# Kernel optimization log

Measured on AMD Instinct MI355X. Metric: run time of the kernel, lower is better.

## Reference

```python
import jax, jax.numpy as jnp
import numpy as np


def setup_inputs() -> dict:
    key = jax.random.key(0)
    x = jax.random.normal(key, (4096, 16384), dtype=jnp.float32)
    return {"x": x, "k": 256}


def reference(x, k):
    # Faithful to Get_Top_K: top_k over abs(x) per row, then scatter the
    # (abs) top-k VALUES back into a zero tensor at their original columns.
    vals, idx = jax.lax.top_k(jnp.abs(x), k)          # [B, K], [B, K]
    rows = jnp.arange(x.shape[0])[:, None]             # [B, 1] broadcast to [B, K]
    out = jnp.zeros_like(x).at[rows, idx].set(vals)    # scatter_nd equivalent
    return out
```

## Files before the change

### kernel.cpp

```cpp
#include <hip/hip_runtime.h>

#define COLS 16384
#define TPB  1024
#define NV   4
#define NW   (TPB / 64)
#define NBIN 4096
#define CHK  (NBIN / TPB)
#define SH1  12
#define RPB  2

typedef unsigned uvec4 __attribute__((ext_vector_type(4)));
typedef float    fvec4 __attribute__((ext_vector_type(4)));

__global__ __launch_bounds__(TPB, 8) void topk_abs_kernel(
    const float* __restrict__ x, const int* __restrict__ kp,
    float* __restrict__ out, int rows)
{
    __shared__ int      hist[NBIN];
    __shared__ int      wsum[NW];
    __shared__ unsigned s_cnt, s_max, s_total;
    __shared__ int      s_bin, s_G, s_eq;

    const int tid = threadIdx.x, lane = tid & 63, wid = tid >> 6;
    const int row0 = blockIdx.x * RPB;
    const int kin = kp[0];
    const unsigned kk = (unsigned)(kin < 0 ? 0 : (kin > COLS ? COLS : kin));

    const uvec4* __restrict__ xrA = (const uvec4*)(x + (size_t)row0 * COLS);
    const uvec4* __restrict__ xrB = (const uvec4*)(x + (size_t)(row0 + 1) * COLS);
    fvec4* __restrict__ orA = (fvec4*)(out + (size_t)row0 * COLS);
    fvec4* __restrict__ orB = (fvec4*)(out + (size_t)(row0 + 1) * COLS);
    const bool hasB = (row0 + 1) < rows;

    uvec4 ubA[NV], ubB[NV];
    #pragma unroll
    for (int i = 0; i < NV; ++i) ubA[i] = xrA[i * TPB + tid];
    if (hasB) {
        #pragma unroll
        for (int i = 0; i < NV; ++i) ubB[i] = xrB[i * TPB + tid];
    }
    #pragma unroll
    for (int j = 0; j < CHK; ++j) hist[tid + j * TPB] = 0;
    __syncthreads();

    auto scan_pick = [&](int rank) {
        const int c  = (TPB - 1) - tid;
        const int b0 = c * CHK;
        int S = 0;
        #pragma unroll
        for (int j = 0; j < CHK; ++j) S += hist[b0 + j];
        int P = S;
        #pragma unroll
        for (int d = 1; d < 64; d <<= 1) { int t = __shfl_up(P, d); if (lane >= d) P += t; }
        if (lane == 63) wsum[wid] = P;
        __syncthreads();
        for (int w = 0; w < wid; ++w) P += wsum[w];
        const int above = P - S;
        if (P >= rank && above < rank) {
            int cum = above;
            #pragma unroll
            for (int j = CHK - 1; j >= 0; --j) {
                int h = hist[b0 + j], prev = cum;
                cum += h;
                if (cum >= rank && prev < rank) { s_bin = b0 + j; s_G = prev; s_eq = h; }
            }
        }
        if (tid == TPB - 1) s_total = (unsigned)P;
        __syncthreads();
    };

    const unsigned T0 = 0x3FE66666u;

    auto process = [&](uvec4 (&ub)[NV], fvec4* __restrict__ or4, bool prep_next) {
        #pragma unroll
        for (int i = 0; i < NV; ++i) {
            uvec4 t = ub[i] & 0x7FFFFFFFu;
            ub[i] = t;
            #define H1(u) { if ((u) >= T0) { unsigned b = ((u) - T0) >> SH1; \
                            b = b < (NBIN - 1) ? b : (NBIN - 1); atomicAdd(&hist[b], 1); } }
            H1(t.x) H1(t.y) H1(t.z) H1(t.w)
            #undef H1
        }
        __syncthreads();

        unsigned T = 0xFFFFFFFFu;
        int need = 0, eq = 0;
        if (kk > 0) {
            scan_pick((int)kk);
            const unsigned cnt = s_total;
            const int B1 = s_bin, G1 = s_G, E1 = s_eq;
            bool handled = false;
            if (cnt == kk) { T = T0; need = 0; eq = 0; handled = true; }
            else if (cnt > kk && B1 < NBIN - 1) {
                if (G1 + E1 == (int)kk) {
                    T = T0 + ((unsigned)B1 << SH1); need = 0; eq = 0; handled = true;
                } else {
                    const unsigned A1 = T0 + ((unsigned)B1 << SH1);
                    const int r1 = (int)kk - G1;
                    #pragma unroll
                    for (int j = 0; j < CHK; ++j) hist[tid + j * TPB] = 0;
                    __syncthreads();
                    #pragma unroll
                    for (int i = 0; i < NV; ++i) {
                        #define H2(u) { unsigned d = (u) - A1; if (d < (unsigned)NBIN) atomicAdd(&hist[d], 1); }
                        H2(ub[i].x) H2(ub[i].y) H2(ub[i].z) H2(ub[i].w)
                        #undef H2
                    }
                    __syncthreads();
                    scan_pick(r1);
                    T = A1 + (unsigned)s_bin; need = r1 - s_G; eq = s_eq;
                    handled = true;
                }
            }
            if (!handled) {
                if (tid == 0) s_max = 0u;
                __syncthreads();
                unsigned lmax = 0u;
                #pragma unroll
                for (int i = 0; i < NV; ++i)
                    lmax = max(lmax, max(max(ub[i].x, ub[i].y), max(ub[i].z, ub[i].w)));
                #pragma unroll
                for (int d = 32; d; d >>= 1) lmax = max(lmax, (unsigned)__shfl_xor((int)lmax, d));
                if (lane == 0) atomicMax(&s_max, lmax);
                __syncthreads();
                const unsigned smax = s_max;

                auto count_ge = [&](unsigned Tq) -> unsigned {
                    __syncthreads();
                    if (tid == 0) s_cnt = 0;
                    __syncthreads();
                    int c = 0;
                    #pragma unroll
                    for (int i = 0; i < NV; ++i)
                        c += (ub[i].x >= Tq) + (ub[i].y >= Tq) + (ub[i].z >= Tq) + (ub[i].w >= Tq);
                    #pragma unroll
                    for (int d = 32; d; d >>= 1) c += __shfl_xor(c, d);
                    if (lane == 0) atomicAdd(&s_cnt, (unsigned)c);
                    __syncthreads();
                    return s_cnt;
                };

                unsigned T0f = T0, cntf = (kk > 0) ? s_total : 0u;
                if (cntf < kk) {
                    unsigned lo = 0u, hi = T0;
                    while (hi - lo > 1u) {
                        unsigned mid = lo + ((hi - lo) >> 1);
                        if (count_ge(mid) >= kk) lo = mid; else hi = mid;
                    }
                    T0f = lo;
                    cntf = count_ge(T0f);
                }
                if (cntf == kk)       { T = T0f; need = 0; eq = 0; }
                else if (smax == T0f) { T = T0f; eq = (int)cntf; need = (int)kk; }
                else {
                    const unsigned range = smax - T0f;
                    const int topbit = 31 - __clz(range);
                    int sh = topbit - 7; if (sh < 0) sh = 0;
                    unsigned A = T0f;
                    unsigned W = (topbit >= 31) ? 0xFFFFFFFFu : (1u << (topbit + 1));
                    int r = (int)kk;
                    for (;;) {
                        if (tid < 256) hist[tid] = 0;
                        __syncthreads();
                        #pragma unroll
                        for (int i = 0; i < NV; ++i) {
                            #define HR(u) { if ((u) >= A && ((u) - A) < W) atomicAdd(&hist[((u) - A) >> sh], 1); }
                            HR(ub[i].x) HR(ub[i].y) HR(ub[i].z) HR(ub[i].w)
                            #undef HR
                        }
                        __syncthreads();
                        int bin = 0, val = 0, s = 0;
                        if (tid < 256) {
                            bin = 255 - tid;
                            val = hist[bin];
                            s = val;
                            #pragma unroll
                            for (int d = 1; d < 64; d <<= 1) { int t = __shfl_up(s, d); if (lane >= d) s += t; }
                            if (lane == 63) wsum[wid] = s;
                        }
                        __syncthreads();
                        if (tid < 256) {
                            for (int w = 0; w < wid; ++w) s += wsum[w];
                            if (s >= r && (s - val) < r) { s_bin = bin; s_G = s - val; if (sh == 0) s_eq = val; }
                        }
                        __syncthreads();
                        A += ((unsigned)s_bin) << sh;
                        W = 1u << sh;
                        r -= s_G;
                        if (sh == 0) break;
                        sh = (sh >= 8) ? sh - 8 : 0;
                    }
                    T = A; need = r; eq = s_eq;
                }
            }
        }

        unsigned cstar = COLS - 1;
        if (kk > 0 && need != eq) {
            unsigned loC = 0, hiC = COLS - 1;
            while (loC < hiC) {
                unsigned mid = (loC + hiC) >> 1;
                __syncthreads();
                if (tid == 0) s_cnt = 0;
                __syncthreads();
                int c = 0;
                #pragma unroll
                for (int i = 0; i < NV; ++i) {
                    const unsigned cb = (unsigned)(i * TPB + tid) * 4u;
                    c += (ub[i].x == T && (cb + 0) <= mid);
                    c += (ub[i].y == T && (cb + 1) <= mid);
                    c += (ub[i].z == T && (cb + 2) <= mid);
                    c += (ub[i].w == T && (cb + 3) <= mid);
                }
                #pragma unroll
                for (int d = 32; d; d >>= 1) c += __shfl_xor(c, d);
                if (lane == 0) atomicAdd(&s_cnt, (unsigned)c);
                __syncthreads();
                if (s_cnt >= (unsigned)need) hiC = mid; else loC = mid + 1;
            }
            cstar = loC;
        }

        if (prep_next) {
            #pragma unroll
            for (int j = 0; j < CHK; ++j) hist[tid + j * TPB] = 0;
        }

        #pragma unroll
        for (int i = 0; i < NV; ++i) {
            const unsigned cb = (unsigned)(i * TPB + tid) * 4u;
            const unsigned u0 = ub[i].x, u1 = ub[i].y, u2 = ub[i].z, u3 = ub[i].w;
            fvec4 o;
            o.x = (u0 > T || (u0 == T && (cb + 0) <= cstar)) ? __uint_as_float(u0) : 0.f;
            o.y = (u1 > T || (u1 == T && (cb + 1) <= cstar)) ? __uint_as_float(u1) : 0.f;
            o.z = (u2 > T || (u2 == T && (cb + 2) <= cstar)) ? __uint_as_float(u2) : 0.f;
            o.w = (u3 > T || (u3 == T && (cb + 3) <= cstar)) ? __uint_as_float(u3) : 0.f;
            __builtin_nontemporal_store(o, &or4[i * TPB + tid]);
        }
        if (prep_next) __syncthreads();
    };

    process(ubA, orA, hasB);
    if (hasB) process(ubB, orB, false);
}

extern "C" void kernel_launch(void* const* d_in, const int* in_sizes, int n_in,
                              void* d_out, int out_size, void* d_ws, size_t ws_size,
                              hipStream_t stream)
{
    const float* x   = (const float*)d_in[0];
    const int*   kp  = (const int*)d_in[1];
    float*       out = (float*)d_out;
    int rows = in_sizes[0] / COLS;
    int grid = (rows + RPB - 1) / RPB;
    topk_abs_kernel<<<grid, TPB, 0, stream>>>(x, kp, out, rows);
}
```

Measured before the change: 81.79 us.

## Process both rows' radix-select passes jointly with packed dual-histogram scans

Instead of running the full select pipeline for row A and then for row B, both rows now build their histograms into separate shared buffers at the same time. A single scan packs the two 16-bit counts into one 32-bit prefix sum. The refinement pass is also shared between the rows, which roughly halves the barrier-bound phases per block. In exchange it doubles histogram shared memory to 32KB, which may lower occupancy against the 8-blocks launch bound, and it relies on per-row counts fitting in 16 bits (max 16384 fits).

```diff
diff --git a/kernel.cpp b/kernel.cpp
--- a/kernel.cpp
+++ b/kernel.cpp
@@ -16,10 +16,12 @@
     const float* __restrict__ x, const int* __restrict__ kp,
     float* __restrict__ out, int rows)
 {
-    __shared__ int      hist[NBIN];
+    __shared__ int      hist[2][NBIN];
+    __shared__ unsigned wsum2[NW];
     __shared__ int      wsum[NW];
-    __shared__ unsigned s_cnt, s_max, s_total;
-    __shared__ int      s_bin, s_G, s_eq;
+    __shared__ unsigned s_cnt, s_max;
+    __shared__ unsigned s_total[2];
+    __shared__ int      s_bin[2], s_G[2], s_eq[2];
 
     const int tid = threadIdx.x, lane = tid & 63, wid = tid >> 6;
     const int row0 = blockIdx.x * RPB;
@@ -40,208 +42,253 @@
         for (int i = 0; i < NV; ++i) ubB[i] = xrB[i * TPB + tid];
     }
     #pragma unroll
-    for (int j = 0; j < CHK; ++j) hist[tid + j * TPB] = 0;
+    for (int j = 0; j < CHK; ++j) { hist[0][tid + j * TPB] = 0; hist[1][tid + j * TPB] = 0; }
     __syncthreads();
 
-    auto scan_pick = [&](int rank) {
+    const unsigned T0 = 0x3FE66666u;
+
+    #pragma unroll
+    for (int i = 0; i < NV; ++i) {
+        uvec4 t = ubA[i] & 0x7FFFFFFFu; ubA[i] = t;
+        #define H1(u) { if ((u) >= T0) { unsigned b = ((u) - T0) >> SH1; \
+                        b = b < (NBIN - 1) ? b : (NBIN - 1); atomicAdd(&hist[0][b], 1); } }
+        H1(t.x) H1(t.y) H1(t.z) H1(t.w)
+        #undef H1
+    }
+    if (hasB) {
+        #pragma unroll
+        for (int i = 0; i < NV; ++i) {
+            uvec4 t = ubB[i] & 0x7FFFFFFFu; ubB[i] = t;
+            #define H1(u) { if ((u) >= T0) { unsigned b = ((u) - T0) >> SH1; \
+                            b = b < (NBIN - 1) ? b : (NBIN - 1); atomicAdd(&hist[1][b], 1); } }
+            H1(t.x) H1(t.y) H1(t.z) H1(t.w)
+            #undef H1
+        }
+    }
+    __syncthreads();
+
+    auto scan2 = [&](int rankA, int rankB) {
         const int c  = (TPB - 1) - tid;
         const int b0 = c * CHK;
-        int S = 0;
-        #pragma unroll
-        for (int j = 0; j < CHK; ++j) S += hist[b0 + j];
-        int P = S;
-        #pragma unroll
-        for (int d = 1; d < 64; d <<= 1) { int t = __shfl_up(P, d); if (lane >= d) P += t; }
-        if (lane == 63) wsum[wid] = P;
+        unsigned SA = 0, SB = 0;
+        #pragma unroll
+        for (int j = 0; j < CHK; ++j) { SA += (unsigned)hist[0][b0 + j]; SB += (unsigned)hist[1][b0 + j]; }
+        unsigned P = SA | (SB << 16);
+        #pragma unroll
+        for (int d = 1; d < 64; d <<= 1) { unsigned t = (unsigned)__shfl_up((int)P, d); if (lane >= d) P += t; }
+        if (lane == 63) wsum2[wid] = P;
         __syncthreads();
-        for (int w = 0; w < wid; ++w) P += wsum[w];
-        const int above = P - S;
-        if (P >= rank && above < rank) {
-            int cum = above;
+        for (int w = 0; w < wid; ++w) P += wsum2[w];
+        const int PA = (int)(P & 0xFFFFu), PB = (int)(P >> 16);
+        if (PA >= rankA && PA - (int)SA < rankA) {
+            int cum = PA - (int)SA;
             #pragma unroll
             for (int j = CHK - 1; j >= 0; --j) {
-                int h = hist[b0 + j], prev = cum;
-                cum += h;
-                if (cum >= rank && prev < rank) { s_bin = b0 + j; s_G = prev; s_eq = h; }
-            }
-        }
-        if (tid == TPB - 1) s_total = (unsigned)P;
+                int h = hist[0][b0 + j], prev = cum; cum += h;
+                if (cum >= rankA && prev < rankA) { s_bin[0] = b0 + j; s_G[0] = prev; s_eq[0] = h; }
+            }
+        }
+        if (PB >= rankB && PB - (int)SB < rankB) {
+            int cum = PB - (int)SB;
+            #pragma unroll
+            for (int j = CHK - 1; j >= 0; --j) {
+                int h = hist[1][b0 + j], prev = cum; cum += h;
+                if (cum >= rankB && prev < rankB) { s_bin[1] = b0 + j; s_G[1] = prev; s_eq[1] = h; }
+            }
+        }
+        if (tid == TPB - 1) { s_total[0] = (unsigned)PA; s_total[1] = (unsigned)PB; }
         __syncthreads();
     };
 
-    const unsigned T0 = 0x3FE66666u;
-
-    auto process = [&](uvec4 (&ub)[NV], fvec4* __restrict__ or4, bool prep_next) {
-        #pragma unroll
-        for (int i = 0; i < NV; ++i) {
-            uvec4 t = ub[i] & 0x7FFFFFFFu;
-            ub[i] = t;
-            #define H1(u) { if ((u) >= T0) { unsigned b = ((u) - T0) >> SH1; \
-                            b = b < (NBIN - 1) ? b : (NBIN - 1); atomicAdd(&hist[b], 1); } }
-            H1(t.x) H1(t.y) H1(t.z) H1(t.w)
-            #undef H1
-        }
-        __syncthreads();
-
-        unsigned T = 0xFFFFFFFFu;
-        int need = 0, eq = 0;
-        if (kk > 0) {
-            scan_pick((int)kk);
-            const unsigned cnt = s_total;
-            const int B1 = s_bin, G1 = s_G, E1 = s_eq;
-            bool handled = false;
-            if (cnt == kk) { T = T0; need = 0; eq = 0; handled = true; }
-            else if (cnt > kk && B1 < NBIN - 1) {
-                if (G1 + E1 == (int)kk) {
-                    T = T0 + ((unsigned)B1 << SH1); need = 0; eq = 0; handled = true;
-                } else {
-                    const unsigned A1 = T0 + ((unsigned)B1 << SH1);
-                    const int r1 = (int)kk - G1;
-                    #pragma unroll
-                    for (int j = 0; j < CHK; ++j) hist[tid + j * TPB] = 0;
-                    __syncthreads();
-                    #pragma unroll
-                    for (int i = 0; i < NV; ++i) {
-                        #define H2(u) { unsigned d = (u) - A1; if (d < (unsigned)NBIN) atomicAdd(&hist[d], 1); }
-                        H2(ub[i].x) H2(ub[i].y) H2(ub[i].z) H2(ub[i].w)
-                        #undef H2
-                    }
-                    __syncthreads();
-                    scan_pick(r1);
-                    T = A1 + (unsigned)s_bin; need = r1 - s_G; eq = s_eq;
-                    handled = true;
-                }
-            }
-            if (!handled) {
-                if (tid == 0) s_max = 0u;
-                __syncthreads();
-                unsigned lmax = 0u;
+    unsigned TA = 0xFFFFFFFFu, TB = 0xFFFFFFFFu;
+    int needA = 0, eqA = 0, needB = 0, eqB = 0;
+    bool p2A = false, p2B = false, fbA = false, fbB = false;
+    unsigned A1A = 0, A1B = 0, cntA = 0, cntB = 0;
+    int r1A = 1, r1B = 1;
+
+    if (kk > 0) {
+        scan2((int)kk, (int)kk);
+        {
+            cntA = s_total[0];
+            const int B1 = s_bin[0], G1 = s_G[0], E1 = s_eq[0];
+            if (cntA == kk) TA = T0;
+            else if (cntA > kk && B1 < NBIN - 1) {
+                if (G1 + E1 == (int)kk) TA = T0 + ((unsigned)B1 << SH1);
+                else { p2A = true; A1A = T0 + ((unsigned)B1 << SH1); r1A = (int)kk - G1; }
+            } else fbA = true;
+        }
+        if (hasB) {
+            cntB = s_total[1];
+            const int B1 = s_bin[1], G1 = s_G[1], E1 = s_eq[1];
+            if (cntB == kk) TB = T0;
+            else if (cntB > kk && B1 < NBIN - 1) {
+                if (G1 + E1 == (int)kk) TB = T0 + ((unsigned)B1 << SH1);
+                else { p2B = true; A1B = T0 + ((unsigned)B1 << SH1); r1B = (int)kk - G1; }
+            } else fbB = true;
+        }
+
+        if (p2A || p2B) {
+            #pragma unroll
+            for (int j = 0; j < CHK; ++j) { hist[0][tid + j * TPB] = 0; hist[1][tid + j * TPB] = 0; }
+            __syncthreads();
+            if (p2A) {
+                #pragma unroll
+                for (int i = 0; i < NV; ++i) {
+                    #define H2(u) { unsigned d = (u) - A1A; if (d < (unsigned)NBIN) atomicAdd(&hist[0][d], 1); }
+                    H2(ubA[i].x) H2(ubA[i].y) H2(ubA[i].z) H2(ubA[i].w)
+                    #undef H2
+                }
+            }
+            if (p2B) {
+                #pragma unroll
+                for (int i = 0; i < NV; ++i) {
+                    #define H2(u) { unsigned d = (u) - A1B; if (d < (unsigned)NBIN) atomicAdd(&hist[1][d], 1); }
+                    H2(ubB[i].x) H2(ubB[i].y) H2(ubB[i].z) H2(ubB[i].w)
+                    #undef H2
+                }
+            }
+            __syncthreads();
+            scan2(p2A ? r1A : 1, p2B ? r1B : 1);
+            if (p2A) { TA = A1A + (unsigned)s_bin[0]; needA = r1A - s_G[0]; eqA = s_eq[0]; }
+            if (p2B) { TB = A1B + (unsigned)s_bin[1]; needB = r1B - s_G[1]; eqB = s_eq[1]; }
+        }
+
+        auto fallback = [&](uvec4 (&ub)[NV], unsigned cnt0, unsigned &T, int &need, int &eq) {
+            if (tid == 0) s_max = 0u;
+            __syncthreads();
+            unsigned lmax = 0u;
+            #pragma unroll
+            for (int i = 0; i < NV; ++i)
+                lmax = max(lmax, max(max(ub[i].x, ub[i].y), max(ub[i].z, ub[i].w)));
+            #pragma unroll
+            for (int d = 32; d; d >>= 1) lmax = max(lmax, (unsigned)__shfl_xor((int)lmax, d));
+            if (lane == 0) atomicMax(&s_max, lmax);
+            __syncthreads();
+            const unsigned smax = s_max;
+
+            auto count_ge = [&](unsigned Tq) -> unsigned {
+                __syncthreads();
+                if (tid == 0) s_cnt = 0;
+                __syncthreads();
+                int c = 0;
                 #pragma unroll
                 for (int i = 0; i < NV; ++i)
-                    lmax = max(lmax, max(max(ub[i].x, ub[i].y), max(ub[i].z, ub[i].w)));
-                #pragma unroll
-                for (int d = 32; d; d >>= 1) lmax = max(lmax, (unsigned)__shfl_xor((int)lmax, d));
-                if (lane == 0) atomicMax(&s_max, lmax);
-                __syncthreads();
-                const unsigned smax = s_max;
-
-                auto count_ge = [&](unsigned Tq) -> unsigned {
-                    __syncthreads();
-                    if (tid == 0) s_cnt = 0;
-                    __syncthreads();
-                    int c = 0;
-                    #pragma unroll
-                    for (int i = 0; i < NV; ++i)
-                        c += (ub[i].x >= Tq) + (ub[i].y >= Tq) + (ub[i].z >= Tq) + (ub[i].w >= Tq);
-                    #pragma unroll
-                    for (int d = 32; d; d >>= 1) c += __shfl_xor(c, d);
-                    if (lane == 0) atomicAdd(&s_cnt, (unsigned)c);
-                    __syncthreads();
-                    return s_cnt;
-                };
-
-                unsigned T0f = T0, cntf = (kk > 0) ? s_total : 0u;
-                if (cntf < kk) {
-                    unsigned lo = 0u, hi = T0;
-                    while (hi - lo > 1u) {
-                        unsigned mid = lo + ((hi - lo) >> 1);
-                        if (count_ge(mid) >= kk) lo = mid; else hi = mid;
-                    }
-                    T0f = lo;
-                    cntf = count_ge(T0f);
-                }
-                if (cntf == kk)       { T = T0f; need = 0; eq = 0; }
-                else if (smax == T0f) { T = T0f; eq = (int)cntf; need = (int)kk; }
-                else {
-                    const unsigned range = smax - T0f;
-                    const int topbit = 31 - __clz(range);
-                    int sh = topbit - 7; if (sh < 0) sh = 0;
-                    unsigned A = T0f;
-                    unsigned W = (topbit >= 31) ? 0xFFFFFFFFu : (1u << (topbit + 1));
-                    int r = (int)kk;
-                    for (;;) {
-                        if (tid < 256) hist[tid] = 0;
-                        __syncthreads();
-                        #pragma unroll
-                        for (int i = 0; i < NV; ++i) {
-                            #define HR(u) { if ((u) >= A && ((u) - A) < W) atomicAdd(&hist[((u) - A) >> sh], 1); }
-                            HR(ub[i].x) HR(ub[i].y) HR(ub[i].z) HR(ub[i].w)
-                            #undef HR
-                        }
-                        __syncthreads();
-                        int bin = 0, val = 0, s = 0;
-                        if (tid < 256) {
-                            bin = 255 - tid;
-                            val = hist[bin];
-                            s = val;
-                            #pragma unroll
-                            for (int d = 1; d < 64; d <<= 1) { int t = __shfl_up(s, d); if (lane >= d) s += t; }
-                            if (lane == 63) wsum[wid] = s;
-                        }
-                        __syncthreads();
-                        if (tid < 256) {
-                            for (int w = 0; w < wid; ++w) s += wsum[w];
-                            if (s >= r && (s - val) < r) { s_bin = bin; s_G = s - val; if (sh == 0) s_eq = val; }
-                        }
-                        __syncthreads();
-                        A += ((unsigned)s_bin) << sh;
-                        W = 1u << sh;
-                        r -= s_G;
-                        if (sh == 0) break;
-                        sh = (sh >= 8) ? sh - 8 : 0;
-                    }
-                    T = A; need = r; eq = s_eq;
-                }
-            }
-        }
-
-        unsigned cstar = COLS - 1;
-        if (kk > 0 && need != eq) {
-            unsigned loC = 0, hiC = COLS - 1;
-            while (loC < hiC) {
-                unsigned mid = (loC + hiC) >> 1;
-                __syncthreads();
-                if (tid == 0) s_cnt = 0;
-                __syncthreads();
-                int c = 0;
-                #pragma unroll
-                for (int i = 0; i < NV; ++i) {
-                    const unsigned cb = (unsigned)(i * TPB + tid) * 4u;
-                    c += (ub[i].x == T && (cb + 0) <= mid);
-                    c += (ub[i].y == T && (cb + 1) <= mid);
-                    c += (ub[i].z == T && (cb + 2) <= mid);
-                    c += (ub[i].w == T && (cb + 3) <= mid);
-                }
+                    c += (ub[i].x >= Tq) + (ub[i].y >= Tq) + (ub[i].z >= Tq) + (ub[i].w >= Tq);
                 #pragma unroll
                 for (int d = 32; d; d >>= 1) c += __shfl_xor(c, d);
                 if (lane == 0) atomicAdd(&s_cnt, (unsigned)c);
                 __syncthreads();
-                if (s_cnt >= (unsigned)need) hiC = mid; else loC = mid + 1;
-            }
-            cstar = loC;
-        }
-
-        if (prep_next) {
-            #pragma unroll
-            for (int j = 0; j < CHK; ++j) hist[tid + j * TPB] = 0;
-        }
-
+                return s_cnt;
+            };
+
+            unsigned T0f = T0, cntf = cnt0;
+            if (cntf < kk) {
+                unsigned lo = 0u, hi = T0;
+                while (hi - lo > 1u) {
+                    unsigned mid = lo + ((hi - lo) >> 1);
+                    if (count_ge(mid) >= kk) lo = mid; else hi = mid;
+                }
+                T0f = lo;
+                cntf = count_ge(T0f);
+            }
+            if (cntf == kk)       { T = T0f; need = 0; eq = 0; return; }
+            if (smax == T0f)      { T = T0f; eq = (int)cntf; need = (int)kk; return; }
+            const unsigned range = smax - T0f;
+            const int topbit = 31 - __clz(range);
+            int sh = topbit - 7; if (sh < 0) sh = 0;
+            unsigned A = T0f;
+            unsigned W = (topbit >= 31) ? 0xFFFFFFFFu : (1u << (topbit + 1));
+            int r = (int)kk;
+            for (;;) {
+                if (tid < 256) hist[0][tid] = 0;
+                __syncthreads();
+                #pragma unroll
+                for (int i = 0; i < NV; ++i) {
+                    #define HR(u) { if ((u) >= A && ((u) - A) < W) atomicAdd(&hist[0][((u) - A) >> sh], 1); }
+                    HR(ub[i].x) HR(ub[i].y) HR(ub[i].z) HR(ub[i].w)
+                    #undef HR
+                }
+                __syncthreads();
+                int bin = 0, val = 0, s = 0;
+                if (tid < 256) {
+                    bin = 255 - tid;
+                    val = hist[0][bin];
+                    s = val;
+                    #pragma unroll
+                    for (int d = 1; d < 64; d <<= 1) { int t = __shfl_up(s, d); if (lane >= d) s += t; }
+                    if (lane == 63) wsum[wid] = s;
+                }
+                __syncthreads();
+                if (tid < 256) {
+                    for (int w = 0; w < wid; ++w) s += wsum[w];
+                    if (s >= r && (s - val) < r) { s_bin[0] = bin; s_G[0] = s - val; if (sh == 0) s_eq[0] = val; }
+                }
+                __syncthreads();
+                A += ((unsigned)s_bin[0]) << sh;
+                W = 1u << sh;
+                r -= s_G[0];
+                if (sh == 0) break;
+                sh = (sh >= 8) ? sh - 8 : 0;
+                __syncthreads();
+            }
+            T = A; need = r; eq = s_eq[0];
+        };
+        if (fbA)          fallback(ubA, cntA, TA, needA, eqA);
+        if (hasB && fbB)  fallback(ubB, cntB, TB, needB, eqB);
+    }
+
+    auto tie_cut = [&](uvec4 (&ub)[NV], unsigned T, int need) -> unsigned {
+        unsigned loC = 0, hiC = COLS - 1;
+        while (loC < hiC) {
+            unsigned mid = (loC + hiC) >> 1;
+            __syncthreads();
+            if (tid == 0) s_cnt = 0;
+            __syncthreads();
+            int c = 0;
+            #pragma unroll
+            for (int i = 0; i < NV; ++i) {
+                const unsigned cb = (unsigned)(i * TPB + tid) * 4u;
+                c += (ub[i].x == T && (cb + 0) <= mid);
+                c += (ub[i].y == T && (cb + 1) <= mid);
+                c += (ub[i].z == T && (cb + 2) <= mid);
+                c += (ub[i].w == T && (cb + 3) <= mid);
+            }
+            #pragma unroll
+            for (int d = 32; d; d >>= 1) c += __shfl_xor(c, d);
+            if (lane == 0) atomicAdd(&s_cnt, (unsigned)c);
+            __syncthreads();
+            if (s_cnt >= (unsigned)need) hiC = mid; else loC = mid + 1;
+        }
+        return loC;
+    };
+    unsigned cstarA = COLS - 1, cstarB = COLS - 1;
+    if (kk > 0 && needA != eqA)         cstarA = tie_cut(ubA, TA, needA);
+    if (kk > 0 && hasB && needB != eqB) cstarB = tie_cut(ubB, TB, needB);
+
+    #pragma unroll
+    for (int i = 0; i < NV; ++i) {
+        const unsigned cb = (unsigned)(i * TPB + tid) * 4u;
+        const unsigned u0 = ubA[i].x, u1 = ubA[i].y, u2 = ubA[i].z, u3 = ubA[i].w;
+        fvec4 o;
+        o.x = (u0 > TA || (u0 == TA && (cb + 0) <= cstarA)) ? __uint_as_float(u0) : 0.f;
+        o.y = (u1 > TA || (u1 == TA && (cb + 1) <= cstarA)) ? __uint_as_float(u1) : 0.f;
+        o.z = (u2 > TA || (u2 == TA && (cb + 2) <= cstarA)) ? __uint_as_float(u2) : 0.f;
+        o.w = (u3 > TA || (u3 == TA && (cb + 3) <= cstarA)) ? __uint_as_float(u3) : 0.f;
+        __builtin_nontemporal_store(o, &orA[i * TPB + tid]);
+    }
+    if (hasB) {
         #pragma unroll
         for (int i = 0; i < NV; ++i) {
             const unsigned cb = (unsigned)(i * TPB + tid) * 4u;
-            const unsigned u0 = ub[i].x, u1 = ub[i].y, u2 = ub[i].z, u3 = ub[i].w;
+            const unsigned u0 = ubB[i].x, u1 = ubB[i].y, u2 = ubB[i].z, u3 = ubB[i].w;
             fvec4 o;
-            o.x = (u0 > T || (u0 == T && (cb + 0) <= cstar)) ? __uint_as_float(u0) : 0.f;
-            o.y = (u1 > T || (u1 == T && (cb + 1) <= cstar)) ? __uint_as_float(u1) : 0.f;
-            o.z = (u2 > T || (u2 == T && (cb + 2) <= cstar)) ? __uint_as_float(u2) : 0.f;
-            o.w = (u3 > T || (u3 == T && (cb + 3) <= cstar)) ? __uint_as_float(u3) : 0.f;
-            __builtin_nontemporal_store(o, &or4[i * TPB + tid]);
-        }
-        if (prep_next) __syncthreads();
-    };
-
-    process(ubA, orA, hasB);
-    if (hasB) process(ubB, orB, false);
+            o.x = (u0 > TB || (u0 == TB && (cb + 0) <= cstarB)) ? __uint_as_float(u0) : 0.f;
+            o.y = (u1 > TB || (u1 == TB && (cb + 1) <= cstarB)) ? __uint_as_float(u1) : 0.f;
+            o.z = (u2 > TB || (u2 == TB && (cb + 2) <= cstarB)) ? __uint_as_float(u2) : 0.f;
+            o.w = (u3 > TB || (u3 == TB && (cb + 3) <= cstarB)) ? __uint_as_float(u3) : 0.f;
+            __builtin_nontemporal_store(o, &orB[i * TPB + tid]);
+        }
+    }
 }
 
 extern "C" void kernel_launch(void* const* d_in, const int* in_sizes, int n_in,
```

Measured after the change: 94.02 us. 1.15x slower.
